# Kernel optimization log

Measured on AMD Instinct MI355X. Metric: run time of the kernel, lower is better.

## Reference

```python
import jax, jax.numpy as jnp
import numpy as np

B, T, S, H, E, V = 32, 32, 64, 512, 512, 32000
NEG = -1e9


def setup_inputs() -> dict:
    key = jax.random.key(0)
    ks = jax.random.split(key, 12)
    g = lambda i, shape: jax.random.normal(ks[i], shape, jnp.float32) * 0.05
    return {
        "tgt_batch": jax.random.randint(ks[0], (B, T), 0, V),
        "len_src_batch": jnp.maximum(jax.random.randint(ks[1], (B,), 0, S), 1),
        "enc_outputs": g(2, (S, B, H)),
        "h0": g(3, (1, B, H)),
        "c0": g(4, (1, B, H)),
        "emb": g(5, (V, E)),
        "W_ih": g(6, (4 * H, E + H)),
        "W_hh": g(7, (4 * H, H)),
        "b_ih": jnp.zeros((4 * H,), jnp.float32),
        "b_hh": jnp.zeros((4 * H,), jnp.float32),
        "W_a": g(8, (H, H)),
        "W_c": g(9, (H, 2 * H)),
        "b_c": jnp.zeros((H,), jnp.float32),
        "W_o": g(10, (V, H)),
        "b_o": jnp.zeros((V,), jnp.float32),
    }


def reference(tgt_batch, len_src_batch, enc_outputs, h0, c0, emb,
              W_ih, W_hh, b_ih, b_hh, W_a, W_c, b_c, W_o, b_o):
    Sv = enc_outputs.shape[0]
    # source padding mask [B,S]
    mask = jnp.arange(Sv)[None, :] < len_src_batch[:, None]
    enc_bsh = enc_outputs.transpose(1, 0, 2)                    # [B,S,H]
    # 'general' attention: score(h,e) = h^T W_a e ; precompute W_a @ e
    proj = jnp.einsum('kh,bsh->bsk', W_a, enc_bsh)              # [B,S,H]
    tgt = tgt_batch.T                                           # [T,B]

    def step(carry, w):
        h, c, ah = carry                                        # each [B,H]
        x = emb[w]                                              # [B,E]
        inp = jnp.concatenate([x, ah], axis=1)                  # [B,E+H]
        gates = inp @ W_ih.T + b_ih + h @ W_hh.T + b_hh         # [B,4H]
        i, f, g, o = jnp.split(gates, 4, axis=1)                # torch gate order
        i, f, o = jax.nn.sigmoid(i), jax.nn.sigmoid(f), jax.nn.sigmoid(o)
        c2 = f * c + i * jnp.tanh(g)
        h2 = o * jnp.tanh(c2)                                   # rnn_output
        scores = jnp.einsum('bk,bsk->bs', h2, proj)
        align = jax.nn.softmax(jnp.where(mask, scores, NEG), axis=1)
        ctx = jnp.einsum('bs,bsh->bh', align, enc_bsh)          # bmm context
        ah2 = jnp.tanh(jnp.concatenate([h2, ctx], axis=1) @ W_c.T + b_c)
        logp = jax.nn.log_softmax(ah2 @ W_o.T + b_o, axis=1)    # [B,V]
        return (h2, c2, ah2), logp

    init = (h0[0], c0[0], jnp.zeros_like(h0[0]))
    _, dec_outputs = jax.lax.scan(step, init, tgt[:-1])         # [T-1,B,V]
    dec_output_words = jnp.argmax(dec_outputs, axis=-1)         # [T-1,B]
    return dec_outputs, dec_output_words
```

## Files before the change

kernel.cpp:

```cpp
#include <hip/hip_runtime.h>
#include <cmath>

#define Bc 32
#define Tc 32
#define Sc 64
#define Hc 512
#define Ec 512
#define Vc 32000
#define NEGC (-1e9f)
#define BH (Bc * Hc)
#define Mtot ((Tc - 1) * Bc)

__device__ __forceinline__ float sigf(float x) { return 1.0f / (1.0f + expf(-x)); }

__device__ __forceinline__ float dot4(const float* a, const float* b) {
    float4 x = *(const float4*)a;
    float4 y = *(const float4*)b;
    return x.x * y.x + x.y * y.y + x.z * y.z + x.w * y.w;
}

__global__ __launch_bounds__(256) void k_init(const float* __restrict__ h0,
                                              const float* __restrict__ c0,
                                              float* __restrict__ h, float* __restrict__ c,
                                              float* __restrict__ ah0) {
    int i = blockIdx.x * 256 + threadIdx.x;
    if (i < BH) { h[i] = h0[i]; c[i] = c0[i]; ah0[i] = 0.0f; }
}

__global__ __launch_bounds__(256) void k_proj(const float* __restrict__ W_a,
                                              const float* __restrict__ enc,
                                              float* __restrict__ proj) {
    int k = blockIdx.x * 256 + threadIdx.x;
    int s0 = blockIdx.y * 8;
    int b = blockIdx.z;
    __shared__ float se[8][Hc];
    for (int i = threadIdx.x; i < 8 * Hc; i += 256) {
        int ss = i >> 9, hh = i & (Hc - 1);
        se[ss][hh] = enc[((size_t)(s0 + ss) * Bc + b) * Hc + hh];
    }
    __syncthreads();
    const float* wr = W_a + (size_t)k * Hc;
    float acc[8];
#pragma unroll
    for (int ss = 0; ss < 8; ++ss) acc[ss] = 0.0f;
    for (int h = 0; h < Hc; h += 4) {
        float4 w = *(const float4*)(wr + h);
#pragma unroll
        for (int ss = 0; ss < 8; ++ss) {
            acc[ss] = fmaf(w.x, se[ss][h + 0], acc[ss]);
            acc[ss] = fmaf(w.y, se[ss][h + 1], acc[ss]);
            acc[ss] = fmaf(w.z, se[ss][h + 2], acc[ss]);
            acc[ss] = fmaf(w.w, se[ss][h + 3], acc[ss]);
        }
    }
#pragma unroll
    for (int ss = 0; ss < 8; ++ss)
        proj[((size_t)b * Sc + s0 + ss) * Hc + k] = acc[ss];
}

__global__ __launch_bounds__(256) void k_step1(const int* __restrict__ tgt,
                                               const float* __restrict__ emb,
                                               const float* __restrict__ W_ih,
                                               const float* __restrict__ W_hh,
                                               const float* __restrict__ b_ih,
                                               const float* __restrict__ b_hh,
                                               const float* __restrict__ h_prev,
                                               const float* __restrict__ c_prev,
                                               const float* __restrict__ ah_prev,
                                               float* __restrict__ h_new,
                                               float* __restrict__ c_new, int t) {
    int tid = threadIdx.x;
    int b = tid & 31;
    int q = (tid >> 5) & 3;
    int hl = tid >> 7;
    int h = blockIdx.x * 2 + hl;
    int j = q * Hc + h;
    int w = tgt[b * Tc + t];
    const float* x = emb + (size_t)w * Ec;
    const float* wi = W_ih + (size_t)j * (Ec + Hc);
    const float* wh = W_hh + (size_t)j * Hc;
    const float* ap = ah_prev + b * Hc;
    const float* hp = h_prev + b * Hc;
    float a0 = 0.f, a1 = 0.f, a2 = 0.f, a3 = 0.f;
    for (int e = 0; e < Ec; e += 16) {
        a0 += dot4(x + e, wi + e);
        a1 += dot4(x + e + 4, wi + e + 4);
        a2 += dot4(x + e + 8, wi + e + 8);
        a3 += dot4(x + e + 12, wi + e + 12);
    }
    for (int k = 0; k < Hc; k += 16) {
        a0 += dot4(ap + k, wi + Ec + k);
        a1 += dot4(ap + k + 4, wi + Ec + k + 4);
        a2 += dot4(ap + k + 8, wi + Ec + k + 8);
        a3 += dot4(ap + k + 12, wi + Ec + k + 12);
    }
    for (int k = 0; k < Hc; k += 16) {
        a0 += dot4(hp + k, wh + k);
        a1 += dot4(hp + k + 4, wh + k + 4);
        a2 += dot4(hp + k + 8, wh + k + 8);
        a3 += dot4(hp + k + 12, wh + k + 12);
    }
    float acc = b_ih[j] + b_hh[j] + ((a0 + a1) + (a2 + a3));

    __shared__ float sg[2][4][32];
    sg[hl][q][b] = acc;
    __syncthreads();
    if (q == 0) {
        float iv = sigf(sg[hl][0][b]);
        float fv = sigf(sg[hl][1][b]);
        float gv = tanhf(sg[hl][2][b]);
        float ov = sigf(sg[hl][3][b]);
        int idx = b * Hc + h;
        float c2 = fv * c_prev[idx] + iv * gv;
        float h2 = ov * tanhf(c2);
        c_new[idx] = c2;
        h_new[idx] = h2;
    }
}

__global__ __launch_bounds__(256) void k_score(const float* __restrict__ proj,
                                               const float* __restrict__ h2,
                                               const int* __restrict__ len_src,
                                               float* __restrict__ align) {
    int b = blockIdx.x;
    int tid = threadIdx.x;
    __shared__ float sh[Hc];
    __shared__ float ss[Sc];
    for (int k = tid; k < Hc; k += 256) sh[k] = h2[b * Hc + k];
    __syncthreads();
    {
        int s = tid >> 2, r = tid & 3;
        const float* pr = proj + ((size_t)b * Sc + s) * Hc + r * 128;
        const float* hh = sh + r * 128;
        float p0 = 0.f, p1 = 0.f;
        for (int k = 0; k < 128; k += 8) {
            p0 += dot4(hh + k, pr + k);
            p1 += dot4(hh + k + 4, pr + k + 4);
        }
        float p = p0 + p1;
        p += __shfl_xor(p, 1);
        p += __shfl_xor(p, 2);
        if (r == 0) ss[s] = p;
    }
    __syncthreads();
    if (tid < Sc) {
        int len = len_src[b];
        float sc = (tid < len) ? ss[tid] : NEGC;
        float mx = sc;
#pragma unroll
        for (int m = 32; m >= 1; m >>= 1) mx = fmaxf(mx, __shfl_xor(mx, m));
        float p = expf(sc - mx);
        float sum = p;
#pragma unroll
        for (int m = 32; m >= 1; m >>= 1) sum += __shfl_xor(sum, m);
        align[b * Sc + tid] = p / sum;
    }
}

__global__ __launch_bounds__(256) void k_ctx(const float* __restrict__ enc,
                                             const float* __restrict__ align,
                                             float* __restrict__ ctx) {
    int hs = blockIdx.x, b = blockIdx.y;
    int tid = threadIdx.x;
    __shared__ float sal[Sc];
    __shared__ float part[2][128];
    if (tid < Sc) sal[tid] = align[b * Sc + tid];
    __syncthreads();
    int half = tid >> 7;
    int hl = tid & 127;
    int h = hs * 128 + hl;
    float acc = 0.0f;
    for (int s = half * 32; s < half * 32 + 32; ++s)
        acc = fmaf(sal[s], enc[((size_t)s * Bc + b) * Hc + h], acc);
    part[half][hl] = acc;
    __syncthreads();
    if (half == 0) ctx[b * Hc + h] = part[0][hl] + part[1][hl];
}

__global__ __launch_bounds__(256) void k_wc(const float* __restrict__ h2,
                                            const float* __restrict__ ctx,
                                            const float* __restrict__ W_c,
                                            const float* __restrict__ b_c,
                                            float* __restrict__ ah_new) {
    int tid = threadIdx.x;
    int kl = tid >> 5;
    int b = tid & 31;
    int k = blockIdx.x * 8 + kl;
    const float* wc = W_c + (size_t)k * (2 * Hc);
    const float* hp = h2 + b * Hc;
    const float* cp = ctx + b * Hc;
    float a0 = 0.f, a1 = 0.f, a2 = 0.f, a3 = 0.f;
    for (int j = 0; j < Hc; j += 16) {
        a0 += dot4(hp + j, wc + j);
        a1 += dot4(hp + j + 4, wc + j + 4);
        a2 += dot4(hp + j + 8, wc + j + 8);
        a3 += dot4(hp + j + 12, wc + j + 12);
    }
    const float* wc2 = wc + Hc;
    for (int j = 0; j < Hc; j += 16) {
        a0 += dot4(cp + j, wc2 + j);
        a1 += dot4(cp + j + 4, wc2 + j + 4);
        a2 += dot4(cp + j + 8, wc2 + j + 8);
        a3 += dot4(cp + j + 12, wc2 + j + 12);
    }
    ah_new[b * Hc + k] = tanhf(b_c[k] + ((a0 + a1) + (a2 + a3)));
}

__global__ __launch_bounds__(256) void k_biglogits(const float* __restrict__ A,
                                                   const float* __restrict__ W_o,
                                                   const float* __restrict__ b_o,
                                                   float* __restrict__ out) {
    __shared__ float At[32][128];
    __shared__ float Bt[32][128];
    int tid = threadIdx.x;
    int n_base = blockIdx.x * 128;
    int m_base = blockIdx.y * 128;
    int tn = tid & 15, tm = tid >> 4;

    float acc[2][4][2][4];
#pragma unroll
    for (int mg = 0; mg < 2; ++mg)
#pragma unroll
        for (int mi = 0; mi < 4; ++mi)
#pragma unroll
            for (int ng = 0; ng < 2; ++ng)
#pragma unroll
                for (int ni = 0; ni < 4; ++ni) acc[mg][mi][ng][ni] = 0.0f;

    int srow = tid >> 1;
    int koff = (tid & 1) * 16;
    int gm = m_base + srow;
    const float* arow = A + (size_t)gm * Hc + koff;
    const float* brow = W_o + (size_t)(n_base + srow) * Hc + koff;

    for (int kc = 0; kc < Hc; kc += 32) {
        float av[16], bv[16];
#pragma unroll
        for (int i = 0; i < 4; ++i) {
            float4 t4 = (gm < Mtot) ? *(const float4*)(arow + kc + i * 4)
                                    : make_float4(0.f, 0.f, 0.f, 0.f);
            av[i * 4 + 0] = t4.x; av[i * 4 + 1] = t4.y; av[i * 4 + 2] = t4.z; av[i * 4 + 3] = t4.w;
            float4 u4 = *(const float4*)(brow + kc + i * 4);
            bv[i * 4 + 0] = u4.x; bv[i * 4 + 1] = u4.y; bv[i * 4 + 2] = u4.z; bv[i * 4 + 3] = u4.w;
        }
        __syncthreads();
#pragma unroll
        for (int i = 0; i < 16; ++i) {
            At[koff + i][srow] = av[i];
            Bt[koff + i][srow] = bv[i];
        }
        __syncthreads();
#pragma unroll
        for (int k = 0; k < 32; ++k) {
            float4 a0 = *(const float4*)&At[k][tm * 4];
            float4 a1 = *(const float4*)&At[k][64 + tm * 4];
            float4 b0 = *(const float4*)&Bt[k][tn * 4];
            float4 b1 = *(const float4*)&Bt[k][64 + tn * 4];
            float am[2][4] = {{a0.x, a0.y, a0.z, a0.w}, {a1.x, a1.y, a1.z, a1.w}};
            float bn[2][4] = {{b0.x, b0.y, b0.z, b0.w}, {b1.x, b1.y, b1.z, b1.w}};
#pragma unroll
            for (int mg = 0; mg < 2; ++mg)
#pragma unroll
                for (int mi = 0; mi < 4; ++mi)
#pragma unroll
                    for (int ng = 0; ng < 2; ++ng)
#pragma unroll
                        for (int ni = 0; ni < 4; ++ni)
                            acc[mg][mi][ng][ni] = fmaf(am[mg][mi], bn[ng][ni], acc[mg][mi][ng][ni]);
        }
        __syncthreads();
    }

#pragma unroll
    for (int ng = 0; ng < 2; ++ng) {
        int n = n_base + ng * 64 + tn * 4;
        float4 bo = *(const float4*)(b_o + n);
#pragma unroll
        for (int mg = 0; mg < 2; ++mg)
#pragma unroll
            for (int mi = 0; mi < 4; ++mi) {
                int m = m_base + mg * 64 + tm * 4 + mi;
                if (m < Mtot) {
                    float4 v;
                    v.x = acc[mg][mi][ng][0] + bo.x;
                    v.y = acc[mg][mi][ng][1] + bo.y;
                    v.z = acc[mg][mi][ng][2] + bo.z;
                    v.w = acc[mg][mi][ng][3] + bo.w;
                    *(float4*)(out + (size_t)m * Vc + n) = v;
                }
            }
    }
}

__global__ __launch_bounds__(256) void k_reduce_norm(float* __restrict__ out,
                                                     float* __restrict__ words) {
    int m = blockIdx.x, tid = threadIdx.x;
    float* row = out + (size_t)m * Vc;
    float mx = -INFINITY;
    int mi = 0;
    for (int v = tid; v < Vc; v += 256) {
        float x = row[v];
        if (x > mx) { mx = x; mi = v; }
    }
    __shared__ float smx[256];
    __shared__ int smi[256];
    __shared__ float ssum[256];
    smx[tid] = mx; smi[tid] = mi;
    __syncthreads();
    for (int off = 128; off; off >>= 1) {
        if (tid < off) {
            float o = smx[tid + off]; int oi = smi[tid + off];
            if (o > smx[tid] || (o == smx[tid] && oi < smi[tid])) { smx[tid] = o; smi[tid] = oi; }
        }
        __syncthreads();
    }
    float gmx = smx[0];
    float s = 0.0f;
    for (int v = tid; v < Vc; v += 256) s += expf(row[v] - gmx);
    ssum[tid] = s;
    __syncthreads();
    for (int off = 128; off; off >>= 1) {
        if (tid < off) ssum[tid] += ssum[tid + off];
        __syncthreads();
    }
    float lse = gmx + logf(ssum[0]);
    __syncthreads();
    for (int v = tid; v < Vc; v += 256) row[v] -= lse;
    if (tid == 0) words[m] = (float)smi[0];
}

extern "C" void kernel_launch(void* const* d_in, const int* in_sizes, int n_in,
                              void* d_out, int out_size, void* d_ws, size_t ws_size,
                              hipStream_t stream) {
    const int*   tgt     = (const int*)d_in[0];
    const int*   len_src = (const int*)d_in[1];
    const float* enc     = (const float*)d_in[2];
    const float* h0      = (const float*)d_in[3];
    const float* c0      = (const float*)d_in[4];
    const float* emb     = (const float*)d_in[5];
    const float* W_ih    = (const float*)d_in[6];
    const float* W_hh    = (const float*)d_in[7];
    const float* b_ih    = (const float*)d_in[8];
    const float* b_hh    = (const float*)d_in[9];
    const float* W_a     = (const float*)d_in[10];
    const float* W_c     = (const float*)d_in[11];
    const float* b_c     = (const float*)d_in[12];
    const float* W_o     = (const float*)d_in[13];
    const float* b_o     = (const float*)d_in[14];

    float* out = (float*)d_out;
    float* ws = (float*)d_ws;

    float* proj   = ws;
    float* hbuf   = proj + (size_t)Bc * Sc * Hc;
    float* cbuf   = hbuf + 2 * BH;
    float* ah_all = cbuf + 2 * BH;
    float* ctx    = ah_all + 32 * BH;
    float* align  = ctx + BH;
    float* out_words = out + (size_t)(Tc - 1) * Bc * Vc;

    k_init<<<64, 256, 0, stream>>>(h0, c0, hbuf, cbuf, ah_all);
    {
        dim3 g(Hc / 256, Sc / 8, Bc);
        k_proj<<<g, 256, 0, stream>>>(W_a, enc, proj);
    }

    int cur = 0;
    for (int t = 0; t < Tc - 1; ++t) {
        int nxt = 1 - cur;
        float* hP = hbuf + cur * BH; float* hN = hbuf + nxt * BH;
        float* cP = cbuf + cur * BH; float* cN = cbuf + nxt * BH;
        float* aP = ah_all + (size_t)t * BH;
        float* aN = ah_all + (size_t)(t + 1) * BH;

        k_step1<<<Hc / 2, 256, 0, stream>>>(tgt, emb, W_ih, W_hh, b_ih, b_hh,
                                            hP, cP, aP, hN, cN, t);
        k_score<<<Bc, 256, 0, stream>>>(proj, hN, len_src, align);
        {
            dim3 g(4, Bc);
            k_ctx<<<g, 256, 0, stream>>>(enc, align, ctx);
        }
        k_wc<<<64, 256, 0, stream>>>(hN, ctx, W_c, b_c, aN);
        cur = nxt;
    }

    {
        dim3 g(Vc / 128, (Mtot + 127) / 128);
        k_biglogits<<<g, 256, 0, stream>>>(ah_all + BH, W_o, b_o, out);
    }
    k_reduce_norm<<<Mtot, 256, 0, stream>>>(out, out_words);
}
```

Before: 4.109 ms.

## Fuse recurrent decoder steps into one persistent kernel with grid barriers

Replaces the 124 per-timestep kernel launches (LSTM cell, score, context, W_c) with a single persistent 256-block kernel that loops over timesteps and synchronises phases through an atomic global barrier. The cell state stays in registers and the score, context and W_c phases are merged per batch row. The log-softmax reduction also switches to an online max/sum pass, which removes one full read of each logits row. The gain depends on all 256 blocks being co-resident; if they are not, the spin barrier deadlocks, and the barrier itself adds latency at every phase.

After: 4.751 ms. 1.16x slower.

```diff
diff --git a/kernel.cpp b/kernel.cpp
--- a/kernel.cpp
+++ b/kernel.cpp
@@ -10,6 +10,7 @@
 #define NEGC (-1e9f)
 #define BH (Bc * Hc)
 #define Mtot ((Tc - 1) * Bc)
+#define NBLK 256
 
 __device__ __forceinline__ float sigf(float x) { return 1.0f / (1.0f + expf(-x)); }
 
@@ -20,11 +21,12 @@
 }
 
 __global__ __launch_bounds__(256) void k_init(const float* __restrict__ h0,
-                                              const float* __restrict__ c0,
-                                              float* __restrict__ h, float* __restrict__ c,
-                                              float* __restrict__ ah0) {
+                                              float* __restrict__ hG,
+                                              float* __restrict__ ah0,
+                                              unsigned* __restrict__ bar) {
     int i = blockIdx.x * 256 + threadIdx.x;
-    if (i < BH) { h[i] = h0[i]; c[i] = c0[i]; ah0[i] = 0.0f; }
+    if (i < BH) { hG[i] = h0[i]; ah0[i] = 0.0f; }
+    if (i < 64) bar[i] = 0u;
 }
 
 __global__ __launch_bounds__(256) void k_proj(const float* __restrict__ W_a,
@@ -58,152 +60,166 @@
         proj[((size_t)b * Sc + s0 + ss) * Hc + k] = acc[ss];
 }
 
-__global__ __launch_bounds__(256) void k_step1(const int* __restrict__ tgt,
-                                               const float* __restrict__ emb,
-                                               const float* __restrict__ W_ih,
-                                               const float* __restrict__ W_hh,
-                                               const float* __restrict__ b_ih,
-                                               const float* __restrict__ b_hh,
-                                               const float* __restrict__ h_prev,
-                                               const float* __restrict__ c_prev,
-                                               const float* __restrict__ ah_prev,
-                                               float* __restrict__ h_new,
-                                               float* __restrict__ c_new, int t) {
+#define GBAR(target)                                                                     \
+    do {                                                                                 \
+        __syncthreads();                                                                 \
+        if (tid == 0) {                                                                  \
+            __threadfence();                                                             \
+            __hip_atomic_fetch_add(bar, 1u, __ATOMIC_RELEASE, __HIP_MEMORY_SCOPE_AGENT); \
+            while (__hip_atomic_load(bar, __ATOMIC_ACQUIRE,                              \
+                                     __HIP_MEMORY_SCOPE_AGENT) < (unsigned)(target))     \
+                __builtin_amdgcn_s_sleep(2);                                             \
+        }                                                                                \
+        __syncthreads();                                                                 \
+        __threadfence();                                                                 \
+    } while (0)
+
+__global__ __launch_bounds__(256, 1) void k_loop(const int* __restrict__ tgt,
+                                                 const float* __restrict__ emb,
+                                                 const float* __restrict__ W_ih,
+                                                 const float* __restrict__ W_hh,
+                                                 const float* __restrict__ b_ih,
+                                                 const float* __restrict__ b_hh,
+                                                 const float* __restrict__ proj,
+                                                 const float* __restrict__ enc,
+                                                 const int* __restrict__ len_src,
+                                                 const float* __restrict__ W_c,
+                                                 const float* __restrict__ b_c,
+                                                 const float* __restrict__ c0,
+                                                 float* __restrict__ hG,
+                                                 float* __restrict__ ah_all,
+                                                 unsigned* __restrict__ bar) {
+    int bid = blockIdx.x;
     int tid = threadIdx.x;
-    int b = tid & 31;
+
+    int b1 = tid & 31;
     int q = (tid >> 5) & 3;
     int hl = tid >> 7;
-    int h = blockIdx.x * 2 + hl;
-    int j = q * Hc + h;
-    int w = tgt[b * Tc + t];
-    const float* x = emb + (size_t)w * Ec;
-    const float* wi = W_ih + (size_t)j * (Ec + Hc);
-    const float* wh = W_hh + (size_t)j * Hc;
-    const float* ap = ah_prev + b * Hc;
-    const float* hp = h_prev + b * Hc;
-    float a0 = 0.f, a1 = 0.f, a2 = 0.f, a3 = 0.f;
-    for (int e = 0; e < Ec; e += 16) {
-        a0 += dot4(x + e, wi + e);
-        a1 += dot4(x + e + 4, wi + e + 4);
-        a2 += dot4(x + e + 8, wi + e + 8);
-        a3 += dot4(x + e + 12, wi + e + 12);
-    }
-    for (int k = 0; k < Hc; k += 16) {
-        a0 += dot4(ap + k, wi + Ec + k);
-        a1 += dot4(ap + k + 4, wi + Ec + k + 4);
-        a2 += dot4(ap + k + 8, wi + Ec + k + 8);
-        a3 += dot4(ap + k + 12, wi + Ec + k + 12);
-    }
-    for (int k = 0; k < Hc; k += 16) {
-        a0 += dot4(hp + k, wh + k);
-        a1 += dot4(hp + k + 4, wh + k + 4);
-        a2 += dot4(hp + k + 8, wh + k + 8);
-        a3 += dot4(hp + k + 12, wh + k + 12);
-    }
-    float acc = b_ih[j] + b_hh[j] + ((a0 + a1) + (a2 + a3));
+    int h = bid * 2 + hl;
+    int j = (q << 9) + h;
+    const float* wi  = W_ih + (size_t)j * (Ec + Hc);
+    const float* wi2 = wi + Ec;
+    const float* wh  = W_hh + (size_t)j * Hc;
+    float bias = b_ih[j] + b_hh[j];
+    float c_reg = (q == 0) ? c0[b1 * Hc + h] : 0.0f;
+
+    int b2 = bid & 31;
+    int g = bid >> 5;
 
     __shared__ float sg[2][4][32];
-    sg[hl][q][b] = acc;
-    __syncthreads();
-    if (q == 0) {
-        float iv = sigf(sg[hl][0][b]);
-        float fv = sigf(sg[hl][1][b]);
-        float gv = tanhf(sg[hl][2][b]);
-        float ov = sigf(sg[hl][3][b]);
-        int idx = b * Hc + h;
-        float c2 = fv * c_prev[idx] + iv * gv;
-        float h2 = ov * tanhf(c2);
-        c_new[idx] = c2;
-        h_new[idx] = h2;
-    }
-}
-
-__global__ __launch_bounds__(256) void k_score(const float* __restrict__ proj,
-                                               const float* __restrict__ h2,
-                                               const int* __restrict__ len_src,
-                                               float* __restrict__ align) {
-    int b = blockIdx.x;
-    int tid = threadIdx.x;
-    __shared__ float sh[Hc];
-    __shared__ float ss[Sc];
-    for (int k = tid; k < Hc; k += 256) sh[k] = h2[b * Hc + k];
-    __syncthreads();
-    {
-        int s = tid >> 2, r = tid & 3;
-        const float* pr = proj + ((size_t)b * Sc + s) * Hc + r * 128;
-        const float* hh = sh + r * 128;
-        float p0 = 0.f, p1 = 0.f;
-        for (int k = 0; k < 128; k += 8) {
-            p0 += dot4(hh + k, pr + k);
-            p1 += dot4(hh + k + 4, pr + k + 4);
-        }
-        float p = p0 + p1;
-        p += __shfl_xor(p, 1);
-        p += __shfl_xor(p, 2);
-        if (r == 0) ss[s] = p;
-    }
-    __syncthreads();
-    if (tid < Sc) {
-        int len = len_src[b];
-        float sc = (tid < len) ? ss[tid] : NEGC;
-        float mx = sc;
-#pragma unroll
-        for (int m = 32; m >= 1; m >>= 1) mx = fmaxf(mx, __shfl_xor(mx, m));
-        float p = expf(sc - mx);
-        float sum = p;
-#pragma unroll
-        for (int m = 32; m >= 1; m >>= 1) sum += __shfl_xor(sum, m);
-        align[b * Sc + tid] = p / sum;
-    }
-}
-
-__global__ __launch_bounds__(256) void k_ctx(const float* __restrict__ enc,
-                                             const float* __restrict__ align,
-                                             float* __restrict__ ctx) {
-    int hs = blockIdx.x, b = blockIdx.y;
-    int tid = threadIdx.x;
+    __shared__ float shc[2 * Hc];
+    __shared__ float sraw[Sc];
     __shared__ float sal[Sc];
-    __shared__ float part[2][128];
-    if (tid < Sc) sal[tid] = align[b * Sc + tid];
-    __syncthreads();
-    int half = tid >> 7;
-    int hl = tid & 127;
-    int h = hs * 128 + hl;
-    float acc = 0.0f;
-    for (int s = half * 32; s < half * 32 + 32; ++s)
-        acc = fmaf(sal[s], enc[((size_t)s * Bc + b) * Hc + h], acc);
-    part[half][hl] = acc;
-    __syncthreads();
-    if (half == 0) ctx[b * Hc + h] = part[0][hl] + part[1][hl];
-}
-
-__global__ __launch_bounds__(256) void k_wc(const float* __restrict__ h2,
-                                            const float* __restrict__ ctx,
-                                            const float* __restrict__ W_c,
-                                            const float* __restrict__ b_c,
-                                            float* __restrict__ ah_new) {
-    int tid = threadIdx.x;
-    int kl = tid >> 5;
-    int b = tid & 31;
-    int k = blockIdx.x * 8 + kl;
-    const float* wc = W_c + (size_t)k * (2 * Hc);
-    const float* hp = h2 + b * Hc;
-    const float* cp = ctx + b * Hc;
-    float a0 = 0.f, a1 = 0.f, a2 = 0.f, a3 = 0.f;
-    for (int j = 0; j < Hc; j += 16) {
-        a0 += dot4(hp + j, wc + j);
-        a1 += dot4(hp + j + 4, wc + j + 4);
-        a2 += dot4(hp + j + 8, wc + j + 8);
-        a3 += dot4(hp + j + 12, wc + j + 12);
-    }
-    const float* wc2 = wc + Hc;
-    for (int j = 0; j < Hc; j += 16) {
-        a0 += dot4(cp + j, wc2 + j);
-        a1 += dot4(cp + j + 4, wc2 + j + 4);
-        a2 += dot4(cp + j + 8, wc2 + j + 8);
-        a3 += dot4(cp + j + 12, wc2 + j + 12);
-    }
-    ah_new[b * Hc + k] = tanhf(b_c[k] + ((a0 + a1) + (a2 + a3)));
+
+    for (int t = 0; t < Tc - 1; ++t) {
+        const float* hR = hG + (t & 1) * BH;
+        float* hW = hG + ((t + 1) & 1) * BH;
+
+        {
+            int w = tgt[b1 * Tc + t];
+            const float* x = emb + (size_t)w * Ec;
+            const float* ap = ah_all + (size_t)t * BH + b1 * Hc;
+            const float* hp = hR + b1 * Hc;
+            float a0 = 0.f, a1 = 0.f, a2 = 0.f, a3 = 0.f;
+            for (int e = 0; e < Ec; e += 16) {
+                a0 += dot4(x + e, wi + e);
+                a1 += dot4(x + e + 4, wi + e + 4);
+                a2 += dot4(x + e + 8, wi + e + 8);
+                a3 += dot4(x + e + 12, wi + e + 12);
+            }
+            for (int k = 0; k < Hc; k += 16) {
+                a0 += dot4(ap + k, wi2 + k);
+                a1 += dot4(ap + k + 4, wi2 + k + 4);
+                a2 += dot4(ap + k + 8, wi2 + k + 8);
+                a3 += dot4(ap + k + 12, wi2 + k + 12);
+            }
+            for (int k = 0; k < Hc; k += 16) {
+                a0 += dot4(hp + k, wh + k);
+                a1 += dot4(hp + k + 4, wh + k + 4);
+                a2 += dot4(hp + k + 8, wh + k + 8);
+                a3 += dot4(hp + k + 12, wh + k + 12);
+            }
+            float acc = bias + ((a0 + a1) + (a2 + a3));
+            sg[hl][q][b1] = acc;
+            __syncthreads();
+            if (q == 0) {
+                float iv = sigf(sg[hl][0][b1]);
+                float fv = sigf(sg[hl][1][b1]);
+                float gv = tanhf(sg[hl][2][b1]);
+                float ov = sigf(sg[hl][3][b1]);
+                c_reg = fv * c_reg + iv * gv;
+                hW[b1 * Hc + h] = ov * tanhf(c_reg);
+            }
+        }
+        GBAR((2 * t + 1) * NBLK);
+
+        {
+            for (int k = tid; k < Hc; k += 256) shc[k] = hW[b2 * Hc + k];
+            __syncthreads();
+
+            {
+                int s = tid >> 2, r = tid & 3;
+                const float* pr = proj + ((size_t)b2 * Sc + s) * Hc + r * 128;
+                const float* hh = shc + r * 128;
+                float p0 = 0.f, p1 = 0.f;
+                for (int k = 0; k < 128; k += 8) {
+                    p0 += dot4(hh + k, pr + k);
+                    p1 += dot4(hh + k + 4, pr + k + 4);
+                }
+                float p = p0 + p1;
+                p += __shfl_xor(p, 1);
+                p += __shfl_xor(p, 2);
+                if (r == 0) sraw[s] = p;
+            }
+            __syncthreads();
+
+            if (tid < Sc) {
+                int len = len_src[b2];
+                float sc = (tid < len) ? sraw[tid] : NEGC;
+                float mx = sc;
+#pragma unroll
+                for (int m = 32; m >= 1; m >>= 1) mx = fmaxf(mx, __shfl_xor(mx, m));
+                float p = expf(sc - mx);
+                float sum = p;
+#pragma unroll
+                for (int m = 32; m >= 1; m >>= 1) sum += __shfl_xor(sum, m);
+                sal[tid] = p / sum;
+            }
+            __syncthreads();
+
+            for (int hh2 = tid; hh2 < Hc; hh2 += 256) {
+                float e0 = 0.f, e1 = 0.f, e2 = 0.f, e3 = 0.f;
+                for (int s = 0; s < Sc; s += 4) {
+                    e0 = fmaf(sal[s + 0], enc[((size_t)(s + 0) * Bc + b2) * Hc + hh2], e0);
+                    e1 = fmaf(sal[s + 1], enc[((size_t)(s + 1) * Bc + b2) * Hc + hh2], e1);
+                    e2 = fmaf(sal[s + 2], enc[((size_t)(s + 2) * Bc + b2) * Hc + hh2], e2);
+                    e3 = fmaf(sal[s + 3], enc[((size_t)(s + 3) * Bc + b2) * Hc + hh2], e3);
+                }
+                shc[Hc + hh2] = ((e0 + e1) + (e2 + e3));
+            }
+            __syncthreads();
+
+            {
+                int kl = tid >> 2, r = tid & 3;
+                int k = g * 64 + kl;
+                const float* wrow = W_c + (size_t)k * (2 * Hc) + r * 256;
+                const float* xv = shc + r * 256;
+                float p0 = 0.f, p1 = 0.f, p2 = 0.f, p3 = 0.f;
+                for (int i = 0; i < 256; i += 16) {
+                    p0 += dot4(xv + i, wrow + i);
+                    p1 += dot4(xv + i + 4, wrow + i + 4);
+                    p2 += dot4(xv + i + 8, wrow + i + 8);
+                    p3 += dot4(xv + i + 12, wrow + i + 12);
+                }
+                float p = ((p0 + p1) + (p2 + p3));
+                p += __shfl_xor(p, 1);
+                p += __shfl_xor(p, 2);
+                if (r == 0)
+                    ah_all[(size_t)(t + 1) * BH + b2 * Hc + k] = tanhf(p + b_c[k]);
+            }
+        }
+        if (t < Tc - 2) GBAR((2 * t + 2) * NBLK);
+    }
 }
 
 __global__ __launch_bounds__(256) void k_biglogits(const float* __restrict__ A,
@@ -296,11 +312,16 @@
                                                      float* __restrict__ words) {
     int m = blockIdx.x, tid = threadIdx.x;
     float* row = out + (size_t)m * Vc;
-    float mx = -INFINITY;
+    float mx = -INFINITY, l = 0.0f;
     int mi = 0;
     for (int v = tid; v < Vc; v += 256) {
         float x = row[v];
-        if (x > mx) { mx = x; mi = v; }
+        if (x > mx) {
+            l = l * expf(mx - x) + 1.0f;
+            mx = x; mi = v;
+        } else {
+            l += expf(x - mx);
+        }
     }
     __shared__ float smx[256];
     __shared__ int smi[256];
@@ -315,9 +336,7 @@
         __syncthreads();
     }
     float gmx = smx[0];
-    float s = 0.0f;
-    for (int v = tid; v < Vc; v += 256) s += expf(row[v] - gmx);
-    ssum[tid] = s;
+    ssum[tid] = l * expf(mx - gmx);
     __syncthreads();
     for (int off = 128; off; off >>= 1) {
         if (tid < off) ssum[tid] += ssum[tid + off];
@@ -352,38 +371,18 @@
     float* ws = (float*)d_ws;
 
     float* proj   = ws;
-    float* hbuf   = proj + (size_t)Bc * Sc * Hc;
-    float* cbuf   = hbuf + 2 * BH;
-    float* ah_all = cbuf + 2 * BH;
-    float* ctx    = ah_all + 32 * BH;
-    float* align  = ctx + BH;
+    float* hG     = proj + (size_t)Bc * Sc * Hc;
+    float* ah_all = hG + 2 * BH;
+    unsigned* bar = (unsigned*)(ah_all + 32 * BH);
     float* out_words = out + (size_t)(Tc - 1) * Bc * Vc;
 
-    k_init<<<64, 256, 0, stream>>>(h0, c0, hbuf, cbuf, ah_all);
+    k_init<<<64, 256, 0, stream>>>(h0, hG, ah_all, bar);
     {
         dim3 g(Hc / 256, Sc / 8, Bc);
         k_proj<<<g, 256, 0, stream>>>(W_a, enc, proj);
     }
-
-    int cur = 0;
-    for (int t = 0; t < Tc - 1; ++t) {
-        int nxt = 1 - cur;
-        float* hP = hbuf + cur * BH; float* hN = hbuf + nxt * BH;
-        float* cP = cbuf + cur * BH; float* cN = cbuf + nxt * BH;
-        float* aP = ah_all + (size_t)t * BH;
-        float* aN = ah_all + (size_t)(t + 1) * BH;
-
-        k_step1<<<Hc / 2, 256, 0, stream>>>(tgt, emb, W_ih, W_hh, b_ih, b_hh,
-                                            hP, cP, aP, hN, cN, t);
-        k_score<<<Bc, 256, 0, stream>>>(proj, hN, len_src, align);
-        {
-            dim3 g(4, Bc);
-            k_ctx<<<g, 256, 0, stream>>>(enc, align, ctx);
-        }
-        k_wc<<<64, 256, 0, stream>>>(hN, ctx, W_c, b_c, aN);
-        cur = nxt;
-    }
-
+    k_loop<<<NBLK, 256, 0, stream>>>(tgt, emb, W_ih, W_hh, b_ih, b_hh, proj, enc,
+                                     len_src, W_c, b_c, c0, hG, ah_all, bar);
     {
         dim3 g(Vc / 128, (Mtot + 127) / 128);
         k_biglogits<<<g, 256, 0, stream>>>(ah_all + BH, W_o, b_o, out);
```
